# Kernel optimization log

Hardware: AMD Instinct MI355X
Metric: run time of the kernel (lower is better)

The kernel has to match this reference:

```python
import jax, jax.numpy as jnp
import numpy as np

N = 12288

def setup_inputs() -> dict:
    key = jax.random.key(0)
    k1, k2, k3 = jax.random.split(key, 3)
    params = jax.random.normal(k1, (N,), dtype=jnp.float32)
    r_mask = jax.random.randint(k2, (N,), 0, 2, dtype=jnp.int32)
    ics_mask = jax.random.randint(k3, (N,), 0, 2, dtype=jnp.int32)
    return {"params": params, "r_mask": r_mask, "ics_mask": ics_mask}

def reference(params, r_mask, ics_mask):
    # Original: -diag(params) @ diag(r_mask).float() + diag(ics_mask)
    # Mathematically: diag(ics_mask - params * r_mask), an [N, N] matrix.
    diag_vals = ics_mask.astype(params.dtype) - params * r_mask.astype(params.dtype)
    return jnp.diag(diag_vals)
```

## Files before the change

kernel.cpp:

```cpp
#include <hip/hip_runtime.h>


#define DIAG_N 12288

__global__ __launch_bounds__(256) void diag_scatter_kernel(
    const float* __restrict__ params,
    const int*   __restrict__ r_mask,
    const int*   __restrict__ ics_mask,
    float*       __restrict__ out)
{
    const int i = blockIdx.x * blockDim.x + threadIdx.x;
    if (i < DIAG_N) {
        const float d = (float)ics_mask[i] - params[i] * (float)r_mask[i];
        out[(size_t)i * (DIAG_N + 1)] = d;
    }
}

extern "C" void kernel_launch(void* const* d_in, const int* in_sizes, int n_in,
                              void* d_out, int out_size, void* d_ws, size_t ws_size,
                              hipStream_t stream) {
    const float* params   = (const float*)d_in[0];
    const int*   r_mask   = (const int*)d_in[1];
    const int*   ics_mask = (const int*)d_in[2];
    float*       out      = (float*)d_out;

    hipMemsetAsync(d_out, 0, (size_t)out_size * sizeof(float), stream);

    dim3 grid((DIAG_N + 255) / 256), block(256);
    hipLaunchKernelGGL(diag_scatter_kernel, grid, block, 0, stream,
                       params, r_mask, ics_mask, out);
}
```

Measured before the change: 572.4 us.

## Fuse zero-fill and diagonal write into one vectorized row-fill kernel

Replaces the separate memset plus strided diagonal-scatter kernel with a single kernel. Each block fills one full row with float4 stores and inserts the diagonal value in the correct lane. This removes the separate memset pass and the uncoalesced scattered writes, so the output is written exactly once with wide coalesced stores. Each block now recomputes a single diagonal element, and the grid has 12288 blocks.

```diff
diff --git a/kernel.cpp b/kernel.cpp
--- a/kernel.cpp
+++ b/kernel.cpp
@@ -2,17 +2,35 @@
 
 
 #define DIAG_N 12288
+#define N4_PER_ROW (DIAG_N / 4)
+#define THREADS 256
+#define F4_PER_THREAD (N4_PER_ROW / THREADS)
 
-__global__ __launch_bounds__(256) void diag_scatter_kernel(
+__global__ __launch_bounds__(THREADS) void diag_row_fill(
     const float* __restrict__ params,
     const int*   __restrict__ r_mask,
     const int*   __restrict__ ics_mask,
-    float*       __restrict__ out)
+    float4*      __restrict__ out)
 {
-    const int i = blockIdx.x * blockDim.x + threadIdx.x;
-    if (i < DIAG_N) {
-        const float d = (float)ics_mask[i] - params[i] * (float)r_mask[i];
-        out[(size_t)i * (DIAG_N + 1)] = d;
+    const int row = blockIdx.x;
+    const int t   = threadIdx.x;
+
+    const int   d4   = row >> 2;
+    const int   lane = row & 3;
+    const float d    = (float)ics_mask[row] - params[row] * (float)r_mask[row];
+
+    float4 dv;
+    dv.x = (lane == 0) ? d : 0.f;
+    dv.y = (lane == 1) ? d : 0.f;
+    dv.z = (lane == 2) ? d : 0.f;
+    dv.w = (lane == 3) ? d : 0.f;
+    const float4 z = make_float4(0.f, 0.f, 0.f, 0.f);
+
+    float4* rowp = out + (size_t)row * N4_PER_ROW;
+#pragma unroll
+    for (int k = 0; k < F4_PER_THREAD; ++k) {
+        const int j = t + k * THREADS;
+        rowp[j] = (j == d4) ? dv : z;
     }
 }
 
@@ -22,11 +40,9 @@
     const float* params   = (const float*)d_in[0];
     const int*   r_mask   = (const int*)d_in[1];
     const int*   ics_mask = (const int*)d_in[2];
-    float*       out      = (float*)d_out;
+    float4*      out      = (float4*)d_out;
 
-    hipMemsetAsync(d_out, 0, (size_t)out_size * sizeof(float), stream);
-
-    dim3 grid((DIAG_N + 255) / 256), block(256);
-    hipLaunchKernelGGL(diag_scatter_kernel, grid, block, 0, stream,
+    dim3 grid(DIAG_N), block(THREADS);
+    hipLaunchKernelGGL(diag_row_fill, grid, block, 0, stream,
                        params, r_mask, ics_mask, out);
 }
```

New measurement: 591.0 us. 3.2% more time.
